# Kernel tuning notes

Hardware: AMD Instinct MI355X
Metric: run time of the kernel (lower is better)

The kernel has to match this reference:

```python
import math
import jax, jax.numpy as jnp
from jax import lax
import numpy as np

DN = ('NCHW', 'OIHW', 'NCHW')


def setup_inputs() -> dict:
    key = jax.random.key(0)
    k0, k1, k2, k3, k4, k5 = jax.random.split(key, 6)
    n, c, h, w = 16, 256, 64, 64
    x = jax.random.normal(k0, (n, c, h, w), jnp.float32)
    b1 = math.sqrt(3.0 / h)
    p1 = jax.random.uniform(k1, (h, c // 8), jnp.float32, -b1, b1)          # p_1_w
    p3 = jax.random.normal(k2, (c, 1, 9, 9), jnp.float32) * 0.05            # depthwise conv, groups=c
    p4 = jax.random.normal(k3, (c, 4, 5, 1), jnp.float32) * 0.05            # grouped conv, groups=c//4
    b5 = math.sqrt(3.0 / (c * w // 8))
    p5 = jax.random.uniform(k4, (c // 8, w, 1, 3 * c), jnp.float32, -b5, b5)  # p_5_w
    p6 = jax.random.normal(k5, (c, 1, 1, 3), jnp.float32) * 0.3             # depthwise conv, groups=c
    return {"x": x, "p1": p1, "p3": p3, "p4": p4, "p5": p5, "p6": p6}


def reference(x, p1, p3, p4, p5, p6):
    n, c, h, w = x.shape
    # t_1: einsum 'abcd,ce->abed' contracts h -> (n, c, c//8, w)
    t1 = jnp.einsum('nchw,he->ncew', x, p1)
    # t_2: unfold(x, (3,1), padding=(1,0)) -> (n, c, 3, h, w)
    xp = jnp.pad(x, ((0, 0), (0, 0), (1, 1), (0, 0)))
    t2 = jnp.stack([xp[:, :, k:k + h, :] for k in range(3)], axis=2)
    # p_3: 9x9 depthwise conv over the (c//8, w) 'spatial' map
    t3 = lax.conv_general_dilated(t1, p3, (1, 1), ((4, 4), (4, 4)),
                                  dimension_numbers=DN, feature_group_count=c)
    # p_4: (5,1) conv with groups=c//4
    t4 = lax.conv_general_dilated(t3, p4, (1, 1), ((2, 2), (0, 0)),
                                  dimension_numbers=DN, feature_group_count=c // 4)
    # t_5: einsum 'abcd,cdef->abef' -> (n, c, 1, 3c) -> (n, c, 3c)
    t5 = jnp.einsum('ncew,ewf->ncf', t4, p5[:, :, 0, :])
    # p_6: (1,3) depthwise conv on (n, c, 1, 3c)
    t6 = lax.conv_general_dilated(t5[:, :, None, :], p6, (1, 1), ((0, 0), (1, 1)),
                                  dimension_numbers=DN, feature_group_count=c)[:, :, 0, :]
    # scaled bmm: (n,c,3c) @ (n,3c,h*w) / sqrt(3c)
    out = jnp.einsum('ncf,nfp->ncp', t6, t2.reshape(n, 3 * c, h * w))
    return (out / math.sqrt(3 * c)).reshape(n, c, h, w)
```

## Files before the change

kernel.cpp:

```cpp
#include <hip/hip_runtime.h>

#define NB 16
#define C  256
#define H  64
#define W  64
#define E  32
#define F  768
#define HW 4096
#define K5 2048
#define XROWS 4224

typedef __attribute__((ext_vector_type(2))) float f32x2;
typedef __attribute__((ext_vector_type(4))) float f32x4;
typedef __attribute__((ext_vector_type(16))) float f32x16;
typedef __attribute__((ext_vector_type(8))) short s16x8;

__device__ inline unsigned short to_bf16(float f) {
  union { float f; unsigned u; } v; v.f = f;
  unsigned u = v.u;
  u += 0x7fff + ((u >> 16) & 1);
  return (unsigned short)(u >> 16);
}

__device__ inline float from_bf16(unsigned short s) {
  union { unsigned u; float f; } v; v.u = ((unsigned)s) << 16;
  return v.f;
}

__device__ inline void gload16(const void* g, void* l) {
  __builtin_amdgcn_global_load_lds((const __attribute__((address_space(1))) unsigned int*)g,
                                   (__attribute__((address_space(3))) unsigned int*)l, 16, 0, 0);
}

__global__ __launch_bounds__(192) void k_wp(const float* __restrict__ p3,
                                            float* __restrict__ w3p) {
  const int c = blockIdx.x;
  const int t = threadIdx.x;
  if (t >= 180) return;
  const int i = t / 20, s = t % 20;
  const float* wr = p3 + c * 81 + i * 9;
  float v;
  if (s < 10) {
    int q = s >> 1, e = s & 1;
    v = (q < 4) ? wr[2 * q + e] : (e ? 0.f : wr[8]);
  } else {
    int s2 = s - 10, q = s2 >> 1, e = s2 & 1;
    v = (q == 0) ? (e ? wr[0] : 0.f) : wr[2 * (q - 1) + 1 + e];
  }
  w3p[(size_t)(c * 9 + i) * 20 + s] = v;
}

__global__ __launch_bounds__(256) void k_t13(const float* __restrict__ x,
                                             const float* __restrict__ p1,
                                             const float* __restrict__ w3p,
                                             unsigned short* __restrict__ t3g) {
  const int nc = blockIdx.x;
  const int c = nc & 255;
  const int tid = threadIdx.x;
  const int lane = tid & 63;
  const int wv = tid >> 6;

  __shared__ __align__(16) unsigned short xs[64][64];
  __shared__ __align__(16) float t1s[40][76];

  for (int i = tid; i < 40 * 76; i += 256) (&t1s[0][0])[i] = 0.f;

  s16x8 afr[2][2];
  {
    const int r = lane & 15;
    const int kb = (lane >> 4) * 8;
#pragma unroll
    for (int m = 0; m < 2; ++m)
#pragma unroll
      for (int kc = 0; kc < 2; ++kc) {
        s16x8 tmp;
#pragma unroll
        for (int j = 0; j < 8; ++j)
          tmp[j] = (short)to_bf16(p1[(kc * 32 + kb + j) * 32 + m * 16 + r]);
        afr[m][kc] = tmp;
      }
  }
  {
    const float* xp = x + (size_t)nc * HW;
#pragma unroll
    for (int t = 0; t < 2; ++t) {
      int uid = tid + 256 * t;
      int h = uid >> 3, uc = uid & 7;
      float4 v0 = *(const float4*)(xp + h * 64 + uc * 8);
      float4 v1 = *(const float4*)(xp + h * 64 + uc * 8 + 4);
      unsigned short b[8] = {to_bf16(v0.x), to_bf16(v0.y), to_bf16(v0.z), to_bf16(v0.w),
                             to_bf16(v1.x), to_bf16(v1.y), to_bf16(v1.z), to_bf16(v1.w)};
      *(uint4*)((char*)&xs[0][0] + h * 128 + ((uc ^ ((h >> 3) & 7)) * 16)) = *(const uint4*)b;
    }
  }
  __syncthreads();
  {
    const int wcol = wv * 16 + (lane & 15);
    f32x4 cf[2] = {{0.f, 0.f, 0.f, 0.f}, {0.f, 0.f, 0.f, 0.f}};
#pragma unroll
    for (int kc = 0; kc < 2; ++kc) {
      const int kb = kc * 32 + (lane >> 4) * 8;
      const char* base = (const char*)&xs[0][0] +
                         kb * 128 + (((wcol >> 3) ^ ((kb >> 3) & 7)) * 16) + (wcol & 7) * 2;
      s16x8 bfrag;
#pragma unroll
      for (int j = 0; j < 8; ++j)
        bfrag[j] = *(const short*)(base + j * 128);
      cf[0] = __builtin_amdgcn_mfma_f32_16x16x32_bf16(afr[0][kc], bfrag, cf[0], 0, 0, 0);
      cf[1] = __builtin_amdgcn_mfma_f32_16x16x32_bf16(afr[1][kc], bfrag, cf[1], 0, 0, 0);
    }
#pragma unroll
    for (int m = 0; m < 2; ++m)
#pragma unroll
      for (int q = 0; q < 4; ++q)
        t1s[4 + m * 16 + (lane >> 4) * 4 + q][4 + wcol] = cf[m][q];
  }
  __syncthreads();
  unsigned short* plane = t3g + (size_t)nc * 2304;
  if (tid < 32) {
    static const int zr[4] = {0, 1, 34, 35};
    int row = zr[tid >> 3], col = (tid & 7) * 8;
    uint4 z = make_uint4(0, 0, 0, 0);
    *(uint4*)(plane + row * 64 + col) = z;
  }
  const int e = tid >> 3, w0 = (tid & 7) * 8;
  f32x2 opk[8] = {};
#pragma unroll
  for (int i = 0; i < 9; ++i) {
    const float* r = &t1s[e + i][w0];
    f32x4 v0 = *(const f32x4*)(r);
    f32x4 v1 = *(const f32x4*)(r + 4);
    f32x4 v2 = *(const f32x4*)(r + 8);
    f32x4 v3 = *(const f32x4*)(r + 12);
    f32x2 wa[8];
    wa[0] = __builtin_shufflevector(v0, v0, 0, 1);
    wa[1] = __builtin_shufflevector(v0, v0, 2, 3);
    wa[2] = __builtin_shufflevector(v1, v1, 0, 1);
    wa[3] = __builtin_shufflevector(v1, v1, 2, 3);
    wa[4] = __builtin_shufflevector(v2, v2, 0, 1);
    wa[5] = __builtin_shufflevector(v2, v2, 2, 3);
    wa[6] = __builtin_shufflevector(v3, v3, 0, 1);
    wa[7] = __builtin_shufflevector(v3, v3, 2, 3);
    const f32x2* wp = (const f32x2*)(w3p + (size_t)(c * 9 + i) * 20);
    f32x2 we0 = wp[0], we1 = wp[1], we2 = wp[2], we3 = wp[3], we4 = wp[4];
    f32x2 wo0 = wp[5], wo1 = wp[6], wo2 = wp[7], wo3 = wp[8], wo4 = wp[9];
#pragma unroll
    for (int t = 0; t < 4; ++t) {
      f32x2 aE = opk[2 * t], aO = opk[2 * t + 1];
      aE += wa[t] * we0;
      aE += wa[t + 1] * we1;
      aE += wa[t + 2] * we2;
      aE += wa[t + 3] * we3;
      aE += wa[t + 4] * we4;
      aO += wa[t] * wo0;
      aO += wa[t + 1] * wo1;
      aO += wa[t + 2] * wo2;
      aO += wa[t + 3] * wo3;
      aO += wa[t + 4] * wo4;
      opk[2 * t] = aE;
      opk[2 * t + 1] = aO;
    }
  }
  unsigned short ob[8];
#pragma unroll
  for (int k = 0; k < 8; ++k) ob[k] = to_bf16(opk[k].x + opk[k].y);
  *(uint4*)(plane + (2 + e) * 64 + w0) = *(const uint4*)ob;
}

__global__ __launch_bounds__(256) void k_t4k(const unsigned short* __restrict__ t3g,
                                             const float* __restrict__ p4,
                                             unsigned short* __restrict__ t4b) {
  const int nc = blockIdx.x;
  const int c = nc & 255;
  const int tid = threadIdx.x;
  const int e = tid >> 3, w0 = (tid & 7) * 8;
  const float* w4 = p4 + c * 20;
  float acc[8];
#pragma unroll
  for (int k = 0; k < 8; ++k) acc[k] = 0.f;
#pragma unroll
  for (int ci = 0; ci < 4; ++ci) {
    const unsigned short* plane = t3g + (size_t)((nc & ~3) + ci) * 2304;
#pragma unroll
    for (int u = 0; u < 5; ++u) {
      uint4 v = *(const uint4*)(plane + (e + u) * 64 + w0);
      const unsigned short* vs = (const unsigned short*)&v;
      float wv = w4[ci * 5 + u];
#pragma unroll
      for (int k = 0; k < 8; ++k) acc[k] += from_bf16(vs[k]) * wv;
    }
  }
  unsigned short ob[8];
#pragma unroll
  for (int k = 0; k < 8; ++k) ob[k] = to_bf16(acc[k]);
  *(uint4*)(t4b + (size_t)nc * 2048 + e * 64 + w0) = *(const uint4*)ob;
}

__global__ __launch_bounds__(256) void k_p5t(const float* __restrict__ p5,
                                             unsigned short* __restrict__ p5t) {
  const int f0 = blockIdx.x * 64;
  const int k0 = blockIdx.y * 64;
  const int tid = threadIdx.x;
  __shared__ __align__(16) unsigned short ls[64][264];
  int fl = tid & 63, k4 = tid >> 6;
  for (int i = 0; i < 16; ++i) {
    int kl = k4 * 16 + i;
    ls[fl][kl] = to_bf16(p5[(size_t)(k0 + kl) * F + f0 + fl]);
  }
  __syncthreads();
#pragma unroll
  for (int j = 0; j < 2; ++j) {
    int chunk = tid + 256 * j;
    int row = chunk >> 3, slot = chunk & 7;
    *(uint4*)(p5t + (size_t)(f0 + row) * K5 + k0 + slot * 8) = *(const uint4*)&ls[row][slot * 8];
  }
}

__global__ __launch_bounds__(256) void k_xt(const float* __restrict__ x,
                                            unsigned short* __restrict__ xt) {
  const int hi = blockIdx.x;
  const int n = blockIdx.y;
  const int tid = threadIdx.x;
  unsigned short* dst = xt + ((size_t)n * XROWS + hi * 64) * C;
  if (hi == 0 || hi == 65) {
    uint4 z = make_uint4(0, 0, 0, 0);
    uint4* d4 = (uint4*)dst;
#pragma unroll
    for (int i = 0; i < 8; ++i) d4[tid + 256 * i] = z;
    return;
  }
  const int h = hi - 1;
  __shared__ __align__(16) unsigned short ls[64][264];
  const float* xp = x + ((size_t)n * C) * HW + h * 64;
  int w = tid & 63, c4 = tid >> 6;
  for (int i = 0; i < 64; ++i) {
    int c = c4 * 64 + i;
    ls[w][c] = to_bf16(xp[(size_t)c * HW + w]);
  }
  __syncthreads();
#pragma unroll
  for (int j = 0; j < 8; ++j) {
    int chunk = tid + 256 * j;
    int row = chunk >> 5, slot = chunk & 31;
    *(uint4*)(dst + row * C + slot * 8) = *(const uint4*)&ls[row][slot * 8];
  }
}

__global__ __launch_bounds__(256) void k_t5m(const unsigned short* __restrict__ A,
                                             const unsigned short* __restrict__ Bt,
                                             unsigned short* __restrict__ Cout) {
  const int bid = blockIdx.x;
  const int wg = (bid & 7) * 96 + (bid >> 3);
  const int nt = wg % 12;
  const int mt = wg / 12;
  const int n0 = nt * 64;
  const int m0 = mt * 64;
  const int tid = threadIdx.x;
  const int lane = tid & 63;
  const int wave = tid >> 6;
  const int wm = wave >> 1, wn = wave & 1;
  __shared__ __align__(16) short As[8192];
  __shared__ __align__(16) short Bs[8192];
  f32x16 acc = {};

  for (int k0 = 0; k0 < K5; k0 += 128) {
#pragma unroll
    for (int i = 0; i < 4; ++i) {
      int chunk = i * 256 + tid;
      int r = chunk >> 4, sl = chunk & 15;
      int sw = sl ^ (r & 15);
      gload16((const char*)(A + (size_t)(m0 + r) * K5 + k0) + sw * 16,
              (char*)As + chunk * 16);
      gload16((const char*)(Bt + (size_t)(n0 + r) * K5 + k0) + sw * 16,
              (char*)Bs + chunk * 16);
    }
    __syncthreads();
#pragma unroll
    for (int kq = 0; kq < 8; ++kq) {
      int arow = wm * 32 + (lane & 31);
      int aslot = (kq * 2 + (lane >> 5)) ^ (arow & 15);
      s16x8 af = *(const s16x8*)((const char*)As + arow * 256 + aslot * 16);
      int brow = wn * 32 + (lane & 31);
      int bslot = (kq * 2 + (lane >> 5)) ^ (brow & 15);
      s16x8 bf = *(const s16x8*)((const char*)Bs + brow * 256 + bslot * 16);
      acc = __builtin_amdgcn_mfma_f32_32x32x16_bf16(af, bf, acc, 0, 0, 0);
    }
    __syncthreads();
  }
  const int col = n0 + wn * 32 + (lane & 31);
#pragma unroll
  for (int r = 0; r < 16; ++r) {
    int grow = m0 + wm * 32 + (r & 3) + 8 * (r >> 2) + 4 * (lane >> 5);
    Cout[(size_t)grow * F + col] = to_bf16(acc[r]);
  }
}

__global__ __launch_bounds__(256) void k_t6(const unsigned short* __restrict__ t5b,
                                            const float* __restrict__ p6,
                                            unsigned short* __restrict__ t6b) {
  int idx = blockIdx.x * 256 + threadIdx.x;
  if (idx >= NB * C * F) return;
  int fp = idx % F;
  int nc = idx / F;
  int c = nc & 255;
  int c2 = fp & 255;
  int kk = fp >> 8;
  int f = 3 * c2 + kk;
  const unsigned short* row = t5b + (size_t)nc * F;
  const float* wt = p6 + c * 3;
  float acc = from_bf16(row[f]) * wt[1];
  if (f > 0) acc += from_bf16(row[f - 1]) * wt[0];
  if (f < F - 1) acc += from_bf16(row[f + 1]) * wt[2];
  t6b[idx] = to_bf16(acc * 0.03608439182435161f);
}

__global__ __launch_bounds__(512, 4) void k_outm(const unsigned short* __restrict__ t6b,
                                                 const unsigned short* __restrict__ xt,
                                                 float* __restrict__ outp) {
  const int bid = blockIdx.x;
  const int wg = (bid & 7) * 64 + (bid >> 3);
  const int n  = wg >> 5;
  const int tile = wg & 31;
  const int p0 = (tile & 15) * 256;
  const int m0 = (tile >> 4) * 128;
  const int tid = threadIdx.x;
  const int lane = tid & 63;
  const int wid = tid >> 6;
  const int wm = wid >> 2;
  const int wn = wid & 3;
  __shared__ __align__(16) short As[8192];
  __shared__ __align__(16) short Bs[16384];
  f32x16 acc[2][2] = {};
  const unsigned short* Abase = t6b + (size_t)(n * C) * F + m0 * F;
  const unsigned short* Xbase = xt + (size_t)n * XROWS * C;

  for (int kt = 0; kt < 12; ++kt) {
    const int k0 = kt * 64;
    const int kk = k0 >> 8, c20 = k0 & 255;
#pragma unroll
    for (int i = 0; i < 2; ++i) {
      int chunk = i * 512 + tid;
      int r = chunk >> 3, sl = chunk & 7, sw = sl ^ (r & 7);
      gload16((const char*)(Abase + (size_t)r * F + k0) + sw * 16,
              (char*)As + chunk * 16);
    }
#pragma unroll
    for (int i = 0; i < 4; ++i) {
      int chunk = i * 512 + tid;
      int r = chunk >> 3, sl = chunk & 7, sw = sl ^ (r & 7);
      gload16((const char*)(Xbase + (size_t)(p0 + r + (kk << 6)) * C + c20) + sw * 16,
              (char*)Bs + chunk * 16);
    }
    __syncthreads();
#pragma unroll
    for (int kq = 0; kq < 4; ++kq) {
      s16x8 af[2], bf[2];
#pragma unroll
      for (int mi = 0; mi < 2; ++mi) {
        int row = wm * 64 + mi * 32 + (lane & 31);
        int byte = (row * 128 + kq * 32 + ((lane >> 5) * 16)) ^ ((row & 7) << 4);
        af[mi] = *(const s16x8*)((const char*)As + byte);
      }
#pragma unroll
      for (int ni = 0; ni < 2; ++ni) {
        int row = wn * 64 + ni * 32 + (lane & 31);
        int byte = (row * 128 + kq * 32 + ((lane >> 5) * 16)) ^ ((row & 7) << 4);
        bf[ni] = *(const s16x8*)((const char*)Bs + byte);
      }
#pragma unroll
      for (int mi = 0; mi < 2; ++mi)
#pragma unroll
        for (int ni = 0; ni < 2; ++ni)
          acc[mi][ni] = __builtin_amdgcn_mfma_f32_32x32x16_bf16(af[mi], bf[ni], acc[mi][ni], 0, 0, 0);
    }
    __syncthreads();
  }
  float* obase = outp + ((size_t)(n * C) + m0) * HW;
#pragma unroll
  for (int mi = 0; mi < 2; ++mi) {
#pragma unroll
    for (int ni = 0; ni < 2; ++ni) {
      int gcol = p0 + wn * 64 + ni * 32 + (lane & 31);
#pragma unroll
      for (int r = 0; r < 16; ++r) {
        int grow = wm * 64 + mi * 32 + (r & 3) + 8 * (r >> 2) + 4 * (lane >> 5);
        obase[(size_t)grow * HW + gcol] = acc[mi][ni][r];
      }
    }
  }
}

extern "C" void kernel_launch(void* const* d_in, const int* in_sizes, int n_in,
                              void* d_out, int out_size, void* d_ws, size_t ws_size,
                              hipStream_t stream) {
  (void)in_sizes; (void)n_in; (void)out_size; (void)ws_size;
  const float* x  = (const float*)d_in[0];
  const float* p1 = (const float*)d_in[1];
  const float* p3 = (const float*)d_in[2];
  const float* p4 = (const float*)d_in[3];
  const float* p5 = (const float*)d_in[4];
  const float* p6 = (const float*)d_in[5];
  float* out = (float*)d_out;

  char* ws = (char*)d_ws;
  unsigned short* t3g = (unsigned short*)ws;
  unsigned short* t4b = (unsigned short*)(ws + 18874368);
  unsigned short* p5t = (unsigned short*)(ws + 35651584);
  unsigned short* t5b = (unsigned short*)(ws + 38797312);
  float*          w3p = (float*)(ws + 47290368);
  unsigned short* t6b = (unsigned short*)ws;
  unsigned short* xt  = (unsigned short*)(ws + 6291456);

  k_wp <<<dim3(C), 192, 0, stream>>>(p3, w3p);
  k_t13<<<dim3(NB * C), 256, 0, stream>>>(x, p1, w3p, t3g);
  k_t4k<<<dim3(NB * C), 256, 0, stream>>>(t3g, p4, t4b);
  k_p5t<<<dim3(12, 32), 256, 0, stream>>>(p5, p5t);
  k_t5m<<<dim3(768), 256, 0, stream>>>(t4b, p5t, t5b);
  k_t6 <<<dim3((NB * C * F + 255) / 256), 256, 0, stream>>>(t5b, p6, t6b);
  k_xt <<<dim3(66, NB), 256, 0, stream>>>(x, xt);
  k_outm<<<dim3(512), 512, 0, stream>>>(t6b, xt, out);
}
```

Measured before the change: 133.6 us.

## Merge weight-prep kernels, group t4 conv per channel group, shrink output GEMM tile

Merges the p5 transpose and p3 weight repack into a single prep launch, removing one kernel launch. Rewrites the grouped (5,1) conv so each block stages its 4-channel input group in swizzled LDS once and computes all 4 output channels, instead of each channel re-reading all 4 input planes from global memory. Halves the final bmm tile along the pixel dimension (128x128 instead of 128x256) and doubles the grid, with launch bounds raised for higher occupancy. In exchange, each output-GEMM block re-reads the A operand across twice as many blocks and does less MFMA work per LDS load.

New measurement: 137.9 us. 3.2% more time.

```diff
diff --git a/kernel.cpp b/kernel.cpp
--- a/kernel.cpp
+++ b/kernel.cpp
@@ -32,22 +32,43 @@
                                    (__attribute__((address_space(3))) unsigned int*)l, 16, 0, 0);
 }
 
-__global__ __launch_bounds__(192) void k_wp(const float* __restrict__ p3,
-                                            float* __restrict__ w3p) {
-  const int c = blockIdx.x;
-  const int t = threadIdx.x;
-  if (t >= 180) return;
-  const int i = t / 20, s = t % 20;
-  const float* wr = p3 + c * 81 + i * 9;
-  float v;
-  if (s < 10) {
-    int q = s >> 1, e = s & 1;
-    v = (q < 4) ? wr[2 * q + e] : (e ? 0.f : wr[8]);
+__global__ __launch_bounds__(256) void k_prep(const float* __restrict__ p5,
+                                              unsigned short* __restrict__ p5t,
+                                              const float* __restrict__ p3,
+                                              float* __restrict__ w3p) {
+  const int bid = blockIdx.x;
+  const int tid = threadIdx.x;
+  if (bid < 384) {
+    const int f0 = (bid % 12) * 64;
+    const int k0 = (bid / 12) * 64;
+    __shared__ __align__(16) unsigned short ls[64][264];
+    int fl = tid & 63, k4 = tid >> 6;
+    for (int i = 0; i < 16; ++i) {
+      int kl = k4 * 16 + i;
+      ls[fl][kl] = to_bf16(p5[(size_t)(k0 + kl) * F + f0 + fl]);
+    }
+    __syncthreads();
+#pragma unroll
+    for (int j = 0; j < 2; ++j) {
+      int chunk = tid + 256 * j;
+      int row = chunk >> 3, slot = chunk & 7;
+      *(uint4*)(p5t + (size_t)(f0 + row) * K5 + k0 + slot * 8) = *(const uint4*)&ls[row][slot * 8];
+    }
   } else {
-    int s2 = s - 10, q = s2 >> 1, e = s2 & 1;
-    v = (q == 0) ? (e ? wr[0] : 0.f) : wr[2 * (q - 1) + 1 + e];
-  }
-  w3p[(size_t)(c * 9 + i) * 20 + s] = v;
+    const int c = bid - 384;
+    if (tid >= 180) return;
+    const int i = tid / 20, s = tid % 20;
+    const float* wr = p3 + c * 81 + i * 9;
+    float v;
+    if (s < 10) {
+      int q = s >> 1, e = s & 1;
+      v = (q < 4) ? wr[2 * q + e] : (e ? 0.f : wr[8]);
+    } else {
+      int s2 = s - 10, q = s2 >> 1, e = s2 & 1;
+      v = (q == 0) ? (e ? wr[0] : 0.f) : wr[2 * (q - 1) + 1 + e];
+    }
+    w3p[(size_t)(c * 9 + i) * 20 + s] = v;
+  }
 }
 
 __global__ __launch_bounds__(256) void k_t13(const float* __restrict__ x,
@@ -167,52 +188,53 @@
   *(uint4*)(plane + (2 + e) * 64 + w0) = *(const uint4*)ob;
 }
 
-__global__ __launch_bounds__(256) void k_t4k(const unsigned short* __restrict__ t3g,
-                                             const float* __restrict__ p4,
-                                             unsigned short* __restrict__ t4b) {
-  const int nc = blockIdx.x;
-  const int c = nc & 255;
-  const int tid = threadIdx.x;
-  const int e = tid >> 3, w0 = (tid & 7) * 8;
-  const float* w4 = p4 + c * 20;
-  float acc[8];
-#pragma unroll
-  for (int k = 0; k < 8; ++k) acc[k] = 0.f;
+__global__ __launch_bounds__(256) void k_t4kg(const unsigned short* __restrict__ t3g,
+                                              const float* __restrict__ p4,
+                                              unsigned short* __restrict__ t4b) {
+  const int blk = blockIdx.x;
+  const int c0 = (blk & 63) * 4;
+  const int n = blk >> 6;
+  const int tid = threadIdx.x;
+  __shared__ __align__(16) unsigned short t3s[4 * 36 * 64];
+
+  const unsigned short* src = t3g + ((size_t)(n * C + c0)) * 2304;
+  for (int i = tid; i < 1152; i += 256) {
+    int rf = i >> 3, sl = i & 7;
+    int sw = sl ^ (rf & 7);
+    gload16((const char*)src + rf * 128 + sw * 16, (char*)t3s + i * 16);
+  }
+  __syncthreads();
+
+  const int e = tid >> 3, w0q = tid & 7;
+  float acc[4][8];
+#pragma unroll
+  for (int qo = 0; qo < 4; ++qo)
+#pragma unroll
+    for (int k = 0; k < 8; ++k) acc[qo][k] = 0.f;
 #pragma unroll
   for (int ci = 0; ci < 4; ++ci) {
-    const unsigned short* plane = t3g + (size_t)((nc & ~3) + ci) * 2304;
 #pragma unroll
     for (int u = 0; u < 5; ++u) {
-      uint4 v = *(const uint4*)(plane + (e + u) * 64 + w0);
+      int rf = ci * 36 + e + u;
+      uint4 v = *(const uint4*)((const char*)t3s + rf * 128 + ((w0q ^ (rf & 7)) * 16));
       const unsigned short* vs = (const unsigned short*)&v;
-      float wv = w4[ci * 5 + u];
-#pragma unroll
-      for (int k = 0; k < 8; ++k) acc[k] += from_bf16(vs[k]) * wv;
-    }
-  }
-  unsigned short ob[8];
-#pragma unroll
-  for (int k = 0; k < 8; ++k) ob[k] = to_bf16(acc[k]);
-  *(uint4*)(t4b + (size_t)nc * 2048 + e * 64 + w0) = *(const uint4*)ob;
-}
-
-__global__ __launch_bounds__(256) void k_p5t(const float* __restrict__ p5,
-                                             unsigned short* __restrict__ p5t) {
-  const int f0 = blockIdx.x * 64;
-  const int k0 = blockIdx.y * 64;
-  const int tid = threadIdx.x;
-  __shared__ __align__(16) unsigned short ls[64][264];
-  int fl = tid & 63, k4 = tid >> 6;
-  for (int i = 0; i < 16; ++i) {
-    int kl = k4 * 16 + i;
-    ls[fl][kl] = to_bf16(p5[(size_t)(k0 + kl) * F + f0 + fl]);
-  }
-  __syncthreads();
-#pragma unroll
-  for (int j = 0; j < 2; ++j) {
-    int chunk = tid + 256 * j;
-    int row = chunk >> 3, slot = chunk & 7;
-    *(uint4*)(p5t + (size_t)(f0 + row) * K5 + k0 + slot * 8) = *(const uint4*)&ls[row][slot * 8];
+      float vf[8];
+#pragma unroll
+      for (int k = 0; k < 8; ++k) vf[k] = from_bf16(vs[k]);
+#pragma unroll
+      for (int qo = 0; qo < 4; ++qo) {
+        float wv = p4[(c0 + qo) * 20 + ci * 5 + u];
+#pragma unroll
+        for (int k = 0; k < 8; ++k) acc[qo][k] += vf[k] * wv;
+      }
+    }
+  }
+#pragma unroll
+  for (int qo = 0; qo < 4; ++qo) {
+    unsigned short ob[8];
+#pragma unroll
+    for (int k = 0; k < 8; ++k) ob[k] = to_bf16(acc[qo][k]);
+    *(uint4*)(t4b + ((size_t)(n * C + c0 + qo)) * 2048 + e * 64 + w0q * 8) = *(const uint4*)ob;
   }
 }
 
@@ -314,23 +336,23 @@
   t6b[idx] = to_bf16(acc * 0.03608439182435161f);
 }
 
-__global__ __launch_bounds__(512, 4) void k_outm(const unsigned short* __restrict__ t6b,
+__global__ __launch_bounds__(512, 8) void k_outm(const unsigned short* __restrict__ t6b,
                                                  const unsigned short* __restrict__ xt,
                                                  float* __restrict__ outp) {
   const int bid = blockIdx.x;
-  const int wg = (bid & 7) * 64 + (bid >> 3);
-  const int n  = wg >> 5;
-  const int tile = wg & 31;
-  const int p0 = (tile & 15) * 256;
-  const int m0 = (tile >> 4) * 128;
+  const int wg = (bid & 7) * 128 + (bid >> 3);
+  const int n  = wg >> 6;
+  const int tile = wg & 63;
+  const int m0 = (tile >> 5) * 128;
+  const int p0 = (tile & 31) * 128;
   const int tid = threadIdx.x;
   const int lane = tid & 63;
   const int wid = tid >> 6;
   const int wm = wid >> 2;
   const int wn = wid & 3;
   __shared__ __align__(16) short As[8192];
-  __shared__ __align__(16) short Bs[16384];
-  f32x16 acc[2][2] = {};
+  __shared__ __align__(16) short Bs[8192];
+  f32x16 acc[2] = {};
   const unsigned short* Abase = t6b + (size_t)(n * C) * F + m0 * F;
   const unsigned short* Xbase = xt + (size_t)n * XROWS * C;
 
@@ -343,49 +365,38 @@
       int r = chunk >> 3, sl = chunk & 7, sw = sl ^ (r & 7);
       gload16((const char*)(Abase + (size_t)r * F + k0) + sw * 16,
               (char*)As + chunk * 16);
-    }
-#pragma unroll
-    for (int i = 0; i < 4; ++i) {
-      int chunk = i * 512 + tid;
-      int r = chunk >> 3, sl = chunk & 7, sw = sl ^ (r & 7);
       gload16((const char*)(Xbase + (size_t)(p0 + r + (kk << 6)) * C + c20) + sw * 16,
               (char*)Bs + chunk * 16);
     }
     __syncthreads();
 #pragma unroll
     for (int kq = 0; kq < 4; ++kq) {
-      s16x8 af[2], bf[2];
+      s16x8 af[2], bf;
 #pragma unroll
       for (int mi = 0; mi < 2; ++mi) {
         int row = wm * 64 + mi * 32 + (lane & 31);
         int byte = (row * 128 + kq * 32 + ((lane >> 5) * 16)) ^ ((row & 7) << 4);
         af[mi] = *(const s16x8*)((const char*)As + byte);
       }
-#pragma unroll
-      for (int ni = 0; ni < 2; ++ni) {
-        int row = wn * 64 + ni * 32 + (lane & 31);
+      {
+        int row = wn * 32 + (lane & 31);
         int byte = (row * 128 + kq * 32 + ((lane >> 5) * 16)) ^ ((row & 7) << 4);
-        bf[ni] = *(const s16x8*)((const char*)Bs + byte);
+        bf = *(const s16x8*)((const char*)Bs + byte);
       }
 #pragma unroll
       for (int mi = 0; mi < 2; ++mi)
-#pragma unroll
-        for (int ni = 0; ni < 2; ++ni)
-          acc[mi][ni] = __builtin_amdgcn_mfma_f32_32x32x16_bf16(af[mi], bf[ni], acc[mi][ni], 0, 0, 0);
+        acc[mi] = __builtin_amdgcn_mfma_f32_32x32x16_bf16(af[mi], bf, acc[mi], 0, 0, 0);
     }
     __syncthreads();
   }
   float* obase = outp + ((size_t)(n * C) + m0) * HW;
+  const int gcol = p0 + wn * 32 + (lane & 31);
 #pragma unroll
   for (int mi = 0; mi < 2; ++mi) {
 #pragma unroll
-    for (int ni = 0; ni < 2; ++ni) {
-      int gcol = p0 + wn * 64 + ni * 32 + (lane & 31);
-#pragma unroll
-      for (int r = 0; r < 16; ++r) {
-        int grow = wm * 64 + mi * 32 + (r & 3) + 8 * (r >> 2) + 4 * (lane >> 5);
-        obase[(size_t)grow * HW + gcol] = acc[mi][ni][r];
-      }
+    for (int r = 0; r < 16; ++r) {
+      int grow = wm * 64 + mi * 32 + (r & 3) + 8 * (r >> 2) + 4 * (lane >> 5);
+      obase[(size_t)grow * HW + gcol] = acc[mi][r];
     }
   }
 }
@@ -411,12 +422,11 @@
   unsigned short* t6b = (unsigned short*)ws;
   unsigned short* xt  = (unsigned short*)(ws + 6291456);
 
-  k_wp <<<dim3(C), 192, 0, stream>>>(p3, w3p);
-  k_t13<<<dim3(NB * C), 256, 0, stream>>>(x, p1, w3p, t3g);
-  k_t4k<<<dim3(NB * C), 256, 0, stream>>>(t3g, p4, t4b);
-  k_p5t<<<dim3(12, 32), 256, 0, stream>>>(p5, p5t);
-  k_t5m<<<dim3(768), 256, 0, stream>>>(t4b, p5t, t5b);
-  k_t6 <<<dim3((NB * C * F + 255) / 256), 256, 0, stream>>>(t5b, p6, t6b);
-  k_xt <<<dim3(66, NB), 256, 0, stream>>>(x, xt);
-  k_outm<<<dim3(512), 512, 0, stream>>>(t6b, xt, out);
-}
+  k_prep<<<dim3(640), 256, 0, stream>>>(p5, p5t, p3, w3p);
+  k_t13 <<<dim3(NB * C), 256, 0, stream>>>(x, p1, w3p, t3g);
+  k_t4kg<<<dim3(NB * 64), 256, 0, stream>>>(t3g, p4, t4b);
+  k_t5m <<<dim3(768), 256, 0, stream>>>(t4b, p5t, t5b);
+  k_t6  <<<dim3((NB * C * F + 255) / 256), 256, 0, stream>>>(t5b, p6, t6b);
+  k_xt  <<<dim3(66, NB), 256, 0, stream>>>(x, xt);
+  k_outm<<<dim3(1024), 512, 0, stream>>>(t6b, xt, out);
+}
```
